# Optimization experiments

Measured on AMD Instinct MI355X. Metric: run time of the kernel, lower is better.

The kernel has to match this reference:

```python
import jax, jax.numpy as jnp
import numpy as np

DIM = 768
HEADS = 12
HEAD_DIM = DIM // HEADS
SCALE = HEAD_DIM ** -0.5
B = 8
N = 2121   # 1 cls + 1600 + 400 + 100 + 20 text
NT = 20

# token ranges: cls [0,1), x0 [1,1601), x1 [1601,2001), x2 [2001,2101), t [2101,2121)
SLICES = {'cls': (0, 1), 'x0': (1, 1601), 'x1': (1601, 2001), 'x2': (2001, 2101), 't': (2101, 2121)}


def setup_inputs() -> dict:
    key = jax.random.key(0)
    k1, k2, k3, k4 = jax.random.split(key, 4)
    src = jax.random.normal(k1, (B, N, DIM), dtype=jnp.float32)
    visu_mask = jnp.zeros((B, 2101), dtype=bool)   # True = masked out
    text_mask = jnp.zeros((B, NT), dtype=bool)
    w_qkv = jax.random.normal(k2, (DIM, 3 * DIM), dtype=jnp.float32) * 0.02
    w_proj = jax.random.normal(k3, (DIM, DIM), dtype=jnp.float32) * 0.02
    b_proj = jax.random.normal(k4, (DIM,), dtype=jnp.float32) * 0.02
    return {'src': src, 'visu_mask': visu_mask, 'text_mask': text_mask,
            'w_qkv': w_qkv, 'w_proj': w_proj, 'b_proj': b_proj}


def _attn(q, k, v, mask):
    # q: [B,H,Nq,D], k/v: [B,H,Nk,D], mask: [B,Nk] bool (True = masked)
    scores = jnp.einsum('bhqd,bhkd->bhqk', q * SCALE, k)
    scores = jnp.where(mask[:, None, None, :], -jnp.inf, scores)
    p = jax.nn.softmax(scores, axis=-1)
    o = jnp.einsum('bhqk,bhkd->bhqd', p, v)          # [B,H,Nq,D]
    return o.transpose(0, 2, 1, 3).reshape(q.shape[0], q.shape[2], -1)  # [B,Nq,C]


def reference(src, visu_mask, text_mask, w_qkv, w_proj, b_proj):
    qkv = (src @ w_qkv).reshape(B, N, 3, HEADS, HEAD_DIM).transpose(2, 0, 3, 1, 4)
    q, k, v = qkv[0], qkv[1], qkv[2]                  # [B,H,N,D]

    def blk(t, lo, hi):
        return t[:, :, lo:hi, :]

    (c0, c1), (a0, a1), (b0, b1), (d0, d1), (t0, t1) = (
        SLICES['cls'], SLICES['x0'], SLICES['x1'], SLICES['x2'], SLICES['t'])

    x0_mask = visu_mask[:, a0:a1]
    x1_mask = visu_mask[:, b0:b1]
    x2_mask = visu_mask[:, d0:d1]
    full_mask = jnp.concatenate([visu_mask, text_mask], axis=1)   # [B, N]

    # cls attends to everything
    cls = _attn(blk(q, c0, c1), k, v, full_mask)
    # x2 attends to x0+x1+x2+t
    k_x2 = jnp.concatenate([blk(k, a0, a1), blk(k, b0, b1), blk(k, d0, d1), blk(k, t0, t1)], axis=2)
    v_x2 = jnp.concatenate([blk(v, a0, a1), blk(v, b0, b1), blk(v, d0, d1), blk(v, t0, t1)], axis=2)
    m_x2 = jnp.concatenate([x0_mask, x1_mask, x2_mask, text_mask], axis=1)
    x2 = _attn(blk(q, d0, d1), k_x2, v_x2, m_x2)
    # x1 attends to x0+x1+t
    k_x1 = jnp.concatenate([blk(k, a0, a1), blk(k, b0, b1), blk(k, t0, t1)], axis=2)
    v_x1 = jnp.concatenate([blk(v, a0, a1), blk(v, b0, b1), blk(v, t0, t1)], axis=2)
    m_x1 = jnp.concatenate([x0_mask, x1_mask, text_mask], axis=1)
    x1 = _attn(blk(q, b0, b1), k_x1, v_x1, m_x1)
    # x0 attends to x0+t
    k_x0 = jnp.concatenate([blk(k, a0, a1), blk(k, t0, t1)], axis=2)
    v_x0 = jnp.concatenate([blk(v, a0, a1), blk(v, t0, t1)], axis=2)
    m_x0 = jnp.concatenate([x0_mask, text_mask], axis=1)
    x0 = _attn(blk(q, a0, a1), k_x0, v_x0, m_x0)
    # text attends to everything
    t = _attn(blk(q, t0, t1), k, v, full_mask)

    x = jnp.concatenate([cls, x0, x1, x2, t], axis=1)
    return x @ w_proj + b_proj
```

## Files before the change

### kernel.cpp

```cpp
#include <hip/hip_runtime.h>
#include <stdint.h>

typedef short           bf16x8 __attribute__((ext_vector_type(8)));
typedef float           f32x4  __attribute__((ext_vector_type(4)));
typedef float           f32x16 __attribute__((ext_vector_type(16)));
typedef unsigned short  u16;
typedef u16             u16x8  __attribute__((ext_vector_type(8)));
typedef uint32_t        u32;
typedef unsigned long long u64;

#define NB    8
#define NSEQ  2121
#define NPAD  2176
#define MROWS 16968
#define MPAD  17024
#define NH    12

#if __has_builtin(__builtin_amdgcn_exp2f)
#define EXP2F(x) __builtin_amdgcn_exp2f(x)
#else
#define EXP2F(x) exp2f(x)
#endif

#define INVALID_S   (-90000.0f)

__device__ __forceinline__ u16 f2bf(float f) {
  uint32_t u = __float_as_uint(f);
  u += 0x7fffu + ((u >> 16) & 1u);
  return (u16)(u >> 16);
}

__global__ void transpose_cast(const float* __restrict__ in, u16* __restrict__ out,
                               int R, int C, int scale_cols, float scale)
{
  __shared__ float tile[32][33];
  const int c0 = blockIdx.x * 32, r0 = blockIdx.y * 32;
  const int tx = threadIdx.x, ty = threadIdx.y;
#pragma unroll
  for (int i = 0; i < 4; i++) {
    const int r = r0 + ty + i * 8;
    tile[ty + i * 8][tx] = in[(size_t)r * C + c0 + tx];
  }
  __syncthreads();
#pragma unroll
  for (int i = 0; i < 4; i++) {
    const int c = c0 + ty + i * 8;
    float v = tile[tx][ty + i * 8];
    if (c < scale_cols) v *= scale;
    out[(size_t)c * R + r0 + tx] = f2bf(v);
  }
}

__global__ __launch_bounds__(256) void cast_src_bf16(const float* __restrict__ in,
                                                     u16* __restrict__ out)
{
  const size_t i = ((size_t)blockIdx.x * 256 + threadIdx.x) * 8;
  float4 a = *(const float4*)(in + i);
  float4 b = *(const float4*)(in + i + 4);
  u16x8 t;
  t[0] = f2bf(a.x); t[1] = f2bf(a.y); t[2] = f2bf(a.z); t[3] = f2bf(a.w);
  t[4] = f2bf(b.x); t[5] = f2bf(b.y); t[6] = f2bf(b.z); t[7] = f2bf(b.w);
  *(u16x8*)(out + i) = t;
}

__global__ __launch_bounds__(256) void gemm_qkv_kernel(
    const u16* __restrict__ srcb, const u16* __restrict__ wt,
    u16* __restrict__ qk, u16* __restrict__ vt)
{
  __shared__ u16 As[128][40];
  __shared__ u16 Bs[128][40];
  const int tid  = threadIdx.x;
  const int lane = tid & 63, wave = tid >> 6;
  const int wr = wave >> 1, wc = wave & 1;
  const int col = lane & 15, grp = lane >> 4;
  const int m0 = blockIdx.y * 128, n0 = blockIdx.x * 128;
  const int arow = tid >> 1, akoff = (tid & 1) * 16;

  const f32x4 fz = {0.f, 0.f, 0.f, 0.f};
  f32x4 acc[4][4];
#pragma unroll
  for (int i = 0; i < 4; i++)
#pragma unroll
    for (int j = 0; j < 4; j++) acc[i][j] = fz;

  const u16* abase = srcb + (size_t)(m0 + arow) * 768 + akoff;
  const u16* bbase = wt   + (size_t)(n0 + arow) * 768 + akoff;
  u16x8 aa0, aa1, bb0, bb1;
  aa0 = *(const u16x8*)(abase);
  aa1 = *(const u16x8*)(abase + 8);
  bb0 = *(const u16x8*)(bbase);
  bb1 = *(const u16x8*)(bbase + 8);

  for (int kb = 0; kb < 768; kb += 32) {
    *(u16x8*)&As[arow][akoff]     = aa0;
    *(u16x8*)&As[arow][akoff + 8] = aa1;
    *(u16x8*)&Bs[arow][akoff]     = bb0;
    *(u16x8*)&Bs[arow][akoff + 8] = bb1;
    __syncthreads();

    if (kb + 32 < 768) {
      aa0 = *(const u16x8*)(abase + kb + 32);
      aa1 = *(const u16x8*)(abase + kb + 40);
      bb0 = *(const u16x8*)(bbase + kb + 32);
      bb1 = *(const u16x8*)(bbase + kb + 40);
    }

    bf16x8 af[4], bfr[4];
#pragma unroll
    for (int mt = 0; mt < 4; mt++) af[mt]  = *(const bf16x8*)&As[wr * 64 + mt * 16 + col][grp * 8];
#pragma unroll
    for (int nt = 0; nt < 4; nt++) bfr[nt] = *(const bf16x8*)&Bs[wc * 64 + nt * 16 + col][grp * 8];
#pragma unroll
    for (int mt = 0; mt < 4; mt++)
#pragma unroll
      for (int nt = 0; nt < 4; nt++)
        acc[mt][nt] = __builtin_amdgcn_mfma_f32_16x16x32_bf16(af[mt], bfr[nt], acc[mt][nt], 0, 0, 0);
    __syncthreads();
  }

#pragma unroll
  for (int mt = 0; mt < 4; mt++) {
#pragma unroll
    for (int r = 0; r < 4; r++) {
      const int mm = m0 + wr * 64 + mt * 16 + grp * 4 + r;
      if (mm >= MROWS) continue;
      const uint32_t bb = (uint32_t)mm / 2121u;
      const uint32_t nn = (uint32_t)mm - bb * 2121u;
#pragma unroll
      for (int nt = 0; nt < 4; nt++) {
        const int c = n0 + wc * 64 + nt * 16 + col;
        const u16 bits = f2bf(acc[mt][nt][r]);
        if (c < 1536) {
          qk[(size_t)mm * 1536 + c] = bits;
        } else {
          const int hd = c - 1536;
          const int h = hd >> 6, d = hd & 63;
          vt[((size_t)(bb * NH + h) * 64 + d) * NPAD + nn] = bits;
        }
      }
    }
  }
}

__global__ __launch_bounds__(256) void gemm_proj_kernel(
    const u16* __restrict__ A, const u16* __restrict__ Bt,
    const float* __restrict__ bias, float* __restrict__ out)
{
  __shared__ u16 As[128][40];
  __shared__ u16 Bs[128][40];
  const int tid  = threadIdx.x;
  const int lane = tid & 63, wave = tid >> 6;
  const int wr = wave >> 1, wc = wave & 1;
  const int col = lane & 15, grp = lane >> 4;
  const int m0 = blockIdx.y * 128, n0 = blockIdx.x * 128;
  const int arow = tid >> 1, akoff = (tid & 1) * 16;

  const f32x4 fz = {0.f, 0.f, 0.f, 0.f};
  f32x4 acc[4][4];
#pragma unroll
  for (int i = 0; i < 4; i++)
#pragma unroll
    for (int j = 0; j < 4; j++) acc[i][j] = fz;

  const u16* abase = A  + (size_t)(m0 + arow) * 768 + akoff;
  const u16* bbase = Bt + (size_t)(n0 + arow) * 768 + akoff;
  u16x8 aa0, aa1, bb0, bb1;
  aa0 = *(const u16x8*)(abase);
  aa1 = *(const u16x8*)(abase + 8);
  bb0 = *(const u16x8*)(bbase);
  bb1 = *(const u16x8*)(bbase + 8);

  for (int kb = 0; kb < 768; kb += 32) {
    *(u16x8*)&As[arow][akoff]     = aa0;
    *(u16x8*)&As[arow][akoff + 8] = aa1;
    *(u16x8*)&Bs[arow][akoff]     = bb0;
    *(u16x8*)&Bs[arow][akoff + 8] = bb1;
    __syncthreads();

    if (kb + 32 < 768) {
      aa0 = *(const u16x8*)(abase + kb + 32);
      aa1 = *(const u16x8*)(abase + kb + 40);
      bb0 = *(const u16x8*)(bbase + kb + 32);
      bb1 = *(const u16x8*)(bbase + kb + 40);
    }

    bf16x8 af[4], bfr[4];
#pragma unroll
    for (int mt = 0; mt < 4; mt++) af[mt]  = *(const bf16x8*)&As[wr * 64 + mt * 16 + col][grp * 8];
#pragma unroll
    for (int nt = 0; nt < 4; nt++) bfr[nt] = *(const bf16x8*)&Bs[wc * 64 + nt * 16 + col][grp * 8];
#pragma unroll
    for (int mt = 0; mt < 4; mt++)
#pragma unroll
      for (int nt = 0; nt < 4; nt++)
        acc[mt][nt] = __builtin_amdgcn_mfma_f32_16x16x32_bf16(af[mt], bfr[nt], acc[mt][nt], 0, 0, 0);
    __syncthreads();
  }

#pragma unroll
  for (int mt = 0; mt < 4; mt++) {
#pragma unroll
    for (int r = 0; r < 4; r++) {
      const int mm = m0 + wr * 64 + mt * 16 + grp * 4 + r;
      if (mm >= MROWS) continue;
#pragma unroll
      for (int nt = 0; nt < 4; nt++) {
        const int c = n0 + wc * 64 + nt * 16 + col;
        out[(size_t)mm * 768 + c] = acc[mt][nt][r] + bias[c];
      }
    }
  }
}

__global__ __launch_bounds__(512) void attn_kernel(
    const u16* __restrict__ qkbuf, const u16* __restrict__ vt,
    const unsigned char* __restrict__ visu, const unsigned char* __restrict__ text,
    u16* __restrict__ attnout)
{
  __shared__ __align__(16) u16 Ks[2][64][72];
  __shared__ __align__(16) u16 Vs[2][64][72];
  __shared__ __align__(16) u64 mb64[34];
  __shared__ __align__(16) float lduf[8][32];

  const int tid  = threadIdx.x;
  const int lane = tid & 63, wave = tid >> 6;
  const int l31 = lane & 31, h = lane >> 5;

  const int fid = blockIdx.x;
  const int swz = (fid & 7) * 108 + (fid >> 3);
  const int qtile = swz % 9;
  const int bh = swz / 9;
  const int b = bh / NH, hh = bh % NH;
  const int qt0 = qtile * 256;
  const int q0 = qt0 + wave * 32;
  const int qrow = q0 + l31;

  for (int c = wave; c < 34; c += 8) {
    const int key = c * 64 + lane;
    int mb = 1;
    if (key < 2101)      mb = visu[b * 2101 + key] ? 1 : 0;
    else if (key < 2121) mb = text[b * 20 + (key - 2101)] ? 1 : 0;
    const u64 bal = __ballot(mb != 0);
    if (lane == 0) mb64[c] = bal;
  }

  const int qload = (qrow < NSEQ) ? qrow : (NSEQ - 1);
  bf16x8 qf[4];
  {
    const u16* qp = qkbuf + (size_t)(b * NSEQ + qload) * 1536 + hh * 64 + h * 8;
#pragma unroll
    for (int s = 0; s < 4; s++) qf[s] = *(const bf16x8*)(qp + s * 16);
  }

  int ks, ke, ex;
  if (qrow == 0)        { ks = 0; ke = 2121; ex = 0; }
  else if (qrow < 1601) { ks = 1; ke = 1601; ex = 1; }
  else if (qrow < 2001) { ks = 1; ke = 2001; ex = 1; }
  else if (qrow < 2101) { ks = 1; ke = 2121; ex = 0; }
  else if (qrow < 2121) { ks = 0; ke = 2121; ex = 0; }
  else                  { ks = 0; ke = 0;    ex = 0; }

  const int hi = (qt0 + 255 < 2120) ? (qt0 + 255) : 2120;
  int ke_tile, extra;
  if (qt0 == 0 || hi >= 2001) { ke_tile = 2121; extra = 0; }
  else if (hi >= 1601)        { ke_tile = 2001; extra = 1; }
  else                        { ke_tile = 1601; extra = 1; }
  const int nkv = (ke_tile + 63) >> 6;
  const int ntot = nkv + extra;

  f32x16 O0, O1;
#pragma unroll
  for (int i = 0; i < 16; i++) { O0[i] = 0.f; O1[i] = 0.f; }
  float lrun = 0.f;

  const int srow = tid >> 3, skoff = (tid & 7) * 8;
  const size_t vbase = (size_t)(b * NH + hh) * 64 * NPAD;
  const u16* kbase = qkbuf + (size_t)(b * NSEQ + srow) * 1536 + 768 + hh * 64 + skoff;
  const u16* vrow  = vt + vbase + (size_t)srow * NPAD + skoff;

  *(u16x8*)&Ks[0][srow][skoff] = *(const u16x8*)kbase;
  *(u16x8*)&Vs[0][srow][skoff] = *(const u16x8*)vrow;
  __syncthreads();

  u16x8 kpre, vpre;

  for (int it = 0; it < ntot; ++it) {
    const int cur = it & 1;
    const int kv0 = (it < nkv) ? it * 64 : 2096;
    const bool more = (it + 1 < ntot);

    if (more) {
      const int kvn = (it + 1 < nkv) ? (it + 1) * 64 : 2096;
      kpre = *(const u16x8*)(kbase + (size_t)kvn * 1536);
      vpre = *(const u16x8*)(vrow + kvn);
    }

    const int skipl = (kv0 >= ke) && !((ex != 0) && (kv0 < 2121) && (kv0 + 64 > 2101));
    if (!__all(skipl)) {
      f32x16 S0, S1;
#pragma unroll
      for (int i = 0; i < 16; i++) { S0[i] = 0.f; S1[i] = 0.f; }
      __builtin_amdgcn_s_setprio(1);
#pragma unroll
      for (int s = 0; s < 4; s++) {
        const bf16x8 k0 = *(const bf16x8*)&Ks[cur][l31][s * 16 + h * 8];
        const bf16x8 k1 = *(const bf16x8*)&Ks[cur][32 + l31][s * 16 + h * 8];
        S0 = __builtin_amdgcn_mfma_f32_32x32x16_bf16(k0, qf[s], S0, 0, 0, 0);
        S1 = __builtin_amdgcn_mfma_f32_32x32x16_bf16(k1, qf[s], S1, 0, 0, 0);
      }
      __builtin_amdgcn_s_setprio(0);

      const int fastl = (kv0 >= ks) && (kv0 + 64 <= ke);
      const u64 mword = (it < nkv) ? mb64[it] : ((mb64[32] >> 48) | (mb64[33] << 16));
      const bool plain = __all(fastl) && (mword == 0ull);
      if (!plain) {
        const u32 wlo = (u32)mword, whi = (u32)(mword >> 32);
#pragma unroll
        for (int m = 0; m < 4; m++) {
#pragma unroll
          for (int r = 0; r < 4; r++) {
            const int bitpos = 8 * m + 4 * h + r;
            {
              const int key = kv0 + bitpos;
              bool valid = ((key >= ks) && (key < ke)) || ((ex != 0) && (key >= 2101));
              valid = valid && (((wlo >> bitpos) & 1u) == 0u);
              S0[4 * m + r] = valid ? S0[4 * m + r] : INVALID_S;
            }
            {
              const int key = kv0 + 32 + bitpos;
              bool valid = ((key >= ks) && (key < ke)) || ((ex != 0) && (key >= 2101));
              valid = valid && (((whi >> bitpos) & 1u) == 0u);
              S1[4 * m + r] = valid ? S1[4 * m + r] : INVALID_S;
            }
          }
        }
      }

      float ls = 0.f;
#pragma unroll
      for (int i = 0; i < 16; i++) { const float p = EXP2F(S0[i]); S0[i] = p; ls += p; }
#pragma unroll
      for (int i = 0; i < 16; i++) { const float p = EXP2F(S1[i]); S1[i] = p; ls += p; }
      lrun += ls;

      bf16x8 pa[4];
      {
        u32 w[8];
#pragma unroll
        for (int j = 0; j < 8; j++) {
          u32 t;
          asm("v_cvt_pk_bf16_f32 %0, %1, %2" : "=v"(t) : "v"(S0[2 * j]), "v"(S0[2 * j + 1]));
          w[j] = t;
        }
        asm("v_permlane32_swap_b32 %0, %1" : "+v"(w[0]), "+v"(w[2]));
        asm("v_permlane32_swap_b32 %0, %1" : "+v"(w[1]), "+v"(w[3]));
        asm("v_permlane32_swap_b32 %0, %1" : "+v"(w[4]), "+v"(w[6]));
        asm("v_permlane32_swap_b32 %0, %1" : "+v"(w[5]), "+v"(w[7]));
        union { u32 u[4]; bf16x8 v; } f0, f1;
        f0.u[0] = w[0]; f0.u[1] = w[1]; f0.u[2] = w[2]; f0.u[3] = w[3];
        f1.u[0] = w[4]; f1.u[1] = w[5]; f1.u[2] = w[6]; f1.u[3] = w[7];
        pa[0] = f0.v; pa[1] = f1.v;
      }
      {
        u32 w[8];
#pragma unroll
        for (int j = 0; j < 8; j++) {
          u32 t;
          asm("v_cvt_pk_bf16_f32 %0, %1, %2" : "=v"(t) : "v"(S1[2 * j]), "v"(S1[2 * j + 1]));
          w[j] = t;
        }
        asm("v_permlane32_swap_b32 %0, %1" : "+v"(w[0]), "+v"(w[2]));
        asm("v_permlane32_swap_b32 %0, %1" : "+v"(w[1]), "+v"(w[3]));
        asm("v_permlane32_swap_b32 %0, %1" : "+v"(w[4]), "+v"(w[6]));
        asm("v_permlane32_swap_b32 %0, %1" : "+v"(w[5]), "+v"(w[7]));
        union { u32 u[4]; bf16x8 v; } f0, f1;
        f0.u[0] = w[0]; f0.u[1] = w[1]; f0.u[2] = w[2]; f0.u[3] = w[3];
        f1.u[0] = w[4]; f1.u[1] = w[5]; f1.u[2] = w[6]; f1.u[3] = w[7];
        pa[2] = f0.v; pa[3] = f1.v;
      }

      __builtin_amdgcn_s_setprio(1);
#pragma unroll
      for (int ck = 0; ck < 4; ck++) {
        const bf16x8 vf0 = *(const bf16x8*)&Vs[cur][l31][ck * 16 + h * 8];
        const bf16x8 vf1 = *(const bf16x8*)&Vs[cur][32 + l31][ck * 16 + h * 8];
        O0 = __builtin_amdgcn_mfma_f32_32x32x16_bf16(pa[ck], vf0, O0, 0, 0, 0);
        O1 = __builtin_amdgcn_mfma_f32_32x32x16_bf16(pa[ck], vf1, O1, 0, 0, 0);
      }
      __builtin_amdgcn_s_setprio(0);
    }

    if (more) {
      *(u16x8*)&Ks[cur ^ 1][srow][skoff] = kpre;
      *(u16x8*)&Vs[cur ^ 1][srow][skoff] = vpre;
    }
    __syncthreads();
  }

  float ltot = lrun + __shfl_xor(lrun, 32);
  if (h == 0) lduf[wave][l31] = ltot;
#pragma unroll
  for (int m = 0; m < 4; m++) {
    const f32x4 lv = *(const f32x4*)&lduf[wave][8 * m + 4 * h];
#pragma unroll
    for (int r = 0; r < 4; r++) {
      const float linv = (lv[r] > 0.f) ? 1.0f / lv[r] : 0.f;
      const int n = q0 + 8 * m + 4 * h + r;
      if (n >= NSEQ) continue;
      u16* op = attnout + (size_t)(b * NSEQ + n) * 768 + hh * 64 + l31;
      op[0]  = f2bf(O0[4 * m + r] * linv);
      op[32] = f2bf(O1[4 * m + r] * linv);
    }
  }
}

extern "C" void kernel_launch(void* const* d_in, const int* in_sizes, int n_in,
                              void* d_out, int out_size, void* d_ws, size_t ws_size,
                              hipStream_t stream) {
  const float* src  = (const float*)d_in[0];
  const unsigned char* visu = (const unsigned char*)d_in[1];
  const unsigned char* text = (const unsigned char*)d_in[2];
  const float* w_qkv = (const float*)d_in[3];
  const float* w_proj = (const float*)d_in[4];
  const float* b_proj = (const float*)d_in[5];
  float* out = (float*)d_out;

  char* ws = (char*)d_ws;
  size_t off = 0;
  auto alloc = [&](size_t bytes) { char* p = ws + off; off += (bytes + 255) & ~(size_t)255; return p; };
  u16* wqkv_t  = (u16*)alloc((size_t)2304 * 768 * 2);
  u16* wproj_t = (u16*)alloc((size_t)768 * 768 * 2);
  u16* qk      = (u16*)alloc((size_t)MPAD * 1536 * 2);
  u16* vtb     = (u16*)alloc((size_t)NB * NH * 64 * NPAD * 2);
  u16* tmp0    = (u16*)alloc((size_t)MPAD * 768 * 2);
  (void)ws_size; (void)in_sizes; (void)n_in; (void)out_size;

  transpose_cast<<<dim3(2304 / 32, 768 / 32), dim3(32, 8), 0, stream>>>(w_qkv, wqkv_t, 768, 2304, 768, 0.125f * 1.4426950408889634f);
  transpose_cast<<<dim3(768 / 32, 768 / 32), dim3(32, 8), 0, stream>>>(w_proj, wproj_t, 768, 768, 0, 1.0f);
  cast_src_bf16<<<dim3(6363), dim3(256), 0, stream>>>(src, tmp0);
  gemm_qkv_kernel<<<dim3(18, 133), dim3(256), 0, stream>>>(tmp0, wqkv_t, qk, vtb);
  attn_kernel<<<dim3(864), dim3(512), 0, stream>>>(qk, vtb, visu, text, tmp0);
  gemm_proj_kernel<<<dim3(6, 133), dim3(256), 0, stream>>>(tmp0, wproj_t, b_proj, out);
}
```

Baseline: 391.8 us.

## Load K/V fragments directly from global per wave, dropping LDS staging

```diff
diff --git a/kernel.cpp b/kernel.cpp
--- a/kernel.cpp
+++ b/kernel.cpp
@@ -212,30 +212,28 @@
   }
 }
 
-__global__ __launch_bounds__(512) void attn_kernel(
+__global__ __launch_bounds__(256) void attn_kernel(
     const u16* __restrict__ qkbuf, const u16* __restrict__ vt,
     const unsigned char* __restrict__ visu, const unsigned char* __restrict__ text,
     u16* __restrict__ attnout)
 {
-  __shared__ __align__(16) u16 Ks[2][64][72];
-  __shared__ __align__(16) u16 Vs[2][64][72];
   __shared__ __align__(16) u64 mb64[34];
-  __shared__ __align__(16) float lduf[8][32];
+  __shared__ __align__(16) float lduf[4][32];
 
   const int tid  = threadIdx.x;
   const int lane = tid & 63, wave = tid >> 6;
   const int l31 = lane & 31, h = lane >> 5;
 
   const int fid = blockIdx.x;
-  const int swz = (fid & 7) * 108 + (fid >> 3);
-  const int qtile = swz % 9;
-  const int bh = swz / 9;
+  const int swz = (fid & 7) * 204 + (fid >> 3);
+  const int qtile = swz % 17;
+  const int bh = swz / 17;
   const int b = bh / NH, hh = bh % NH;
-  const int qt0 = qtile * 256;
+  const int qt0 = qtile * 128;
   const int q0 = qt0 + wave * 32;
   const int qrow = q0 + l31;
 
-  for (int c = wave; c < 34; c += 8) {
+  for (int c = wave; c < 34; c += 4) {
     const int key = c * 64 + lane;
     int mb = 1;
     if (key < 2101)      mb = visu[b * 2101 + key] ? 1 : 0;
@@ -243,11 +241,11 @@
     const u64 bal = __ballot(mb != 0);
     if (lane == 0) mb64[c] = bal;
   }
-
-  const int qload = (qrow < NSEQ) ? qrow : (NSEQ - 1);
+  __syncthreads();
+
   bf16x8 qf[4];
   {
-    const u16* qp = qkbuf + (size_t)(b * NSEQ + qload) * 1536 + hh * 64 + h * 8;
+    const u16* qp = qkbuf + (size_t)(b * NSEQ + qrow) * 1536 + hh * 64 + h * 8;
 #pragma unroll
     for (int s = 0; s < 4; s++) qf[s] = *(const bf16x8*)(qp + s * 16);
   }
@@ -260,141 +258,133 @@
   else if (qrow < 2121) { ks = 0; ke = 2121; ex = 0; }
   else                  { ks = 0; ke = 0;    ex = 0; }
 
-  const int hi = (qt0 + 255 < 2120) ? (qt0 + 255) : 2120;
-  int ke_tile, extra;
-  if (qt0 == 0 || hi >= 2001) { ke_tile = 2121; extra = 0; }
-  else if (hi >= 1601)        { ke_tile = 2001; extra = 1; }
-  else                        { ke_tile = 1601; extra = 1; }
-  const int nkv = (ke_tile + 63) >> 6;
-  const int ntot = nkv + extra;
+  int ntot, nkv;
+  if (q0 >= NSEQ) {
+    ntot = 0; nkv = 0;
+  } else {
+    const int hi = (q0 + 31 < 2120) ? (q0 + 31) : 2120;
+    int ke_tile, extra;
+    if (q0 == 0 || hi >= 2001) { ke_tile = 2121; extra = 0; }
+    else if (hi >= 1601)       { ke_tile = 2001; extra = 1; }
+    else                       { ke_tile = 1601; extra = 1; }
+    nkv = (ke_tile + 63) >> 6;
+    ntot = nkv + extra;
+  }
 
   f32x16 O0, O1;
 #pragma unroll
   for (int i = 0; i < 16; i++) { O0[i] = 0.f; O1[i] = 0.f; }
   float lrun = 0.f;
 
-  const int srow = tid >> 3, skoff = (tid & 7) * 8;
-  const size_t vbase = (size_t)(b * NH + hh) * 64 * NPAD;
-  const u16* kbase = qkbuf + (size_t)(b * NSEQ + srow) * 1536 + 768 + hh * 64 + skoff;
-  const u16* vrow  = vt + vbase + (size_t)srow * NPAD + skoff;
-
-  *(u16x8*)&Ks[0][srow][skoff] = *(const u16x8*)kbase;
-  *(u16x8*)&Vs[0][srow][skoff] = *(const u16x8*)vrow;
-  __syncthreads();
-
-  u16x8 kpre, vpre;
+  const u16* kp0 = qkbuf + (size_t)(b * NSEQ + l31) * 1536 + 768 + hh * 64 + h * 8;
+  const u16* vp0 = vt + (size_t)(b * NH + hh) * 64 * NPAD + (size_t)l31 * NPAD + h * 8;
 
   for (int it = 0; it < ntot; ++it) {
-    const int cur = it & 1;
     const int kv0 = (it < nkv) ? it * 64 : 2096;
-    const bool more = (it + 1 < ntot);
-
-    if (more) {
-      const int kvn = (it + 1 < nkv) ? (it + 1) * 64 : 2096;
-      kpre = *(const u16x8*)(kbase + (size_t)kvn * 1536);
-      vpre = *(const u16x8*)(vrow + kvn);
-    }
-
-    const int skipl = (kv0 >= ke) && !((ex != 0) && (kv0 < 2121) && (kv0 + 64 > 2101));
-    if (!__all(skipl)) {
-      f32x16 S0, S1;
-#pragma unroll
-      for (int i = 0; i < 16; i++) { S0[i] = 0.f; S1[i] = 0.f; }
-      __builtin_amdgcn_s_setprio(1);
-#pragma unroll
-      for (int s = 0; s < 4; s++) {
-        const bf16x8 k0 = *(const bf16x8*)&Ks[cur][l31][s * 16 + h * 8];
-        const bf16x8 k1 = *(const bf16x8*)&Ks[cur][32 + l31][s * 16 + h * 8];
-        S0 = __builtin_amdgcn_mfma_f32_32x32x16_bf16(k0, qf[s], S0, 0, 0, 0);
-        S1 = __builtin_amdgcn_mfma_f32_32x32x16_bf16(k1, qf[s], S1, 0, 0, 0);
-      }
-      __builtin_amdgcn_s_setprio(0);
-
-      const int fastl = (kv0 >= ks) && (kv0 + 64 <= ke);
-      const u64 mword = (it < nkv) ? mb64[it] : ((mb64[32] >> 48) | (mb64[33] << 16));
-      const bool plain = __all(fastl) && (mword == 0ull);
-      if (!plain) {
-        const u32 wlo = (u32)mword, whi = (u32)(mword >> 32);
-#pragma unroll
-        for (int m = 0; m < 4; m++) {
-#pragma unroll
-          for (int r = 0; r < 4; r++) {
-            const int bitpos = 8 * m + 4 * h + r;
-            {
-              const int key = kv0 + bitpos;
-              bool valid = ((key >= ks) && (key < ke)) || ((ex != 0) && (key >= 2101));
-              valid = valid && (((wlo >> bitpos) & 1u) == 0u);
-              S0[4 * m + r] = valid ? S0[4 * m + r] : INVALID_S;
-            }
-            {
-              const int key = kv0 + 32 + bitpos;
-              bool valid = ((key >= ks) && (key < ke)) || ((ex != 0) && (key >= 2101));
-              valid = valid && (((whi >> bitpos) & 1u) == 0u);
-              S1[4 * m + r] = valid ? S1[4 * m + r] : INVALID_S;
-            }
+
+    const u16* kp = kp0 + (size_t)kv0 * 1536;
+    bf16x8 kf0[4], kf1[4];
+#pragma unroll
+    for (int s = 0; s < 4; s++) {
+      kf0[s] = *(const bf16x8*)(kp + s * 16);
+      kf1[s] = *(const bf16x8*)(kp + (size_t)32 * 1536 + s * 16);
+    }
+
+    f32x16 S0, S1;
+#pragma unroll
+    for (int i = 0; i < 16; i++) { S0[i] = 0.f; S1[i] = 0.f; }
+    __builtin_amdgcn_s_setprio(1);
+#pragma unroll
+    for (int s = 0; s < 4; s++) {
+      S0 = __builtin_amdgcn_mfma_f32_32x32x16_bf16(kf0[s], qf[s], S0, 0, 0, 0);
+      S1 = __builtin_amdgcn_mfma_f32_32x32x16_bf16(kf1[s], qf[s], S1, 0, 0, 0);
+    }
+    __builtin_amdgcn_s_setprio(0);
+
+    const u16* vp = vp0 + kv0;
+    bf16x8 vf0[4], vf1[4];
+#pragma unroll
+    for (int ck = 0; ck < 4; ck++) {
+      vf0[ck] = *(const bf16x8*)(vp + ck * 16);
+      vf1[ck] = *(const bf16x8*)(vp + (size_t)32 * NPAD + ck * 16);
+    }
+
+    const int fastl = (kv0 >= ks) && (kv0 + 64 <= ke);
+    const u64 mword = (it < nkv) ? mb64[it] : ((mb64[32] >> 48) | (mb64[33] << 16));
+    const bool plain = __all(fastl) && (mword == 0ull);
+    if (!plain) {
+      const u32 wlo = (u32)mword, whi = (u32)(mword >> 32);
+#pragma unroll
+      for (int m = 0; m < 4; m++) {
+#pragma unroll
+        for (int r = 0; r < 4; r++) {
+          const int bitpos = 8 * m + 4 * h + r;
+          {
+            const int key = kv0 + bitpos;
+            bool valid = ((key >= ks) && (key < ke)) || ((ex != 0) && (key >= 2101));
+            valid = valid && (((wlo >> bitpos) & 1u) == 0u);
+            S0[4 * m + r] = valid ? S0[4 * m + r] : INVALID_S;
+          }
+          {
+            const int key = kv0 + 32 + bitpos;
+            bool valid = ((key >= ks) && (key < ke)) || ((ex != 0) && (key >= 2101));
+            valid = valid && (((whi >> bitpos) & 1u) == 0u);
+            S1[4 * m + r] = valid ? S1[4 * m + r] : INVALID_S;
           }
         }
       }
-
-      float ls = 0.f;
-#pragma unroll
-      for (int i = 0; i < 16; i++) { const float p = EXP2F(S0[i]); S0[i] = p; ls += p; }
-#pragma unroll
-      for (int i = 0; i < 16; i++) { const float p = EXP2F(S1[i]); S1[i] = p; ls += p; }
-      lrun += ls;
-
-      bf16x8 pa[4];
-      {
-        u32 w[8];
-#pragma unroll
-        for (int j = 0; j < 8; j++) {
-          u32 t;
-          asm("v_cvt_pk_bf16_f32 %0, %1, %2" : "=v"(t) : "v"(S0[2 * j]), "v"(S0[2 * j + 1]));
-          w[j] = t;
-        }
-        asm("v_permlane32_swap_b32 %0, %1" : "+v"(w[0]), "+v"(w[2]));
-        asm("v_permlane32_swap_b32 %0, %1" : "+v"(w[1]), "+v"(w[3]));
-        asm("v_permlane32_swap_b32 %0, %1" : "+v"(w[4]), "+v"(w[6]));
-        asm("v_permlane32_swap_b32 %0, %1" : "+v"(w[5]), "+v"(w[7]));
-        union { u32 u[4]; bf16x8 v; } f0, f1;
-        f0.u[0] = w[0]; f0.u[1] = w[1]; f0.u[2] = w[2]; f0.u[3] = w[3];
-        f1.u[0] = w[4]; f1.u[1] = w[5]; f1.u[2] = w[6]; f1.u[3] = w[7];
-        pa[0] = f0.v; pa[1] = f1.v;
+    }
+
+    float ls = 0.f;
+#pragma unroll
+    for (int i = 0; i < 16; i++) { const float p = EXP2F(S0[i]); S0[i] = p; ls += p; }
+#pragma unroll
+    for (int i = 0; i < 16; i++) { const float p = EXP2F(S1[i]); S1[i] = p; ls += p; }
+    lrun += ls;
+
+    bf16x8 pa[4];
+    {
+      u32 w[8];
+#pragma unroll
+      for (int j = 0; j < 8; j++) {
+        u32 t;
+        asm("v_cvt_pk_bf16_f32 %0, %1, %2" : "=v"(t) : "v"(S0[2 * j]), "v"(S0[2 * j + 1]));
+        w[j] = t;
       }
-      {
-        u32 w[8];
-#pragma unroll
-        for (int j = 0; j < 8; j++) {
-          u32 t;
-          asm("v_cvt_pk_bf16_f32 %0, %1, %2" : "=v"(t) : "v"(S1[2 * j]), "v"(S1[2 * j + 1]));
-          w[j] = t;
-        }
-        asm("v_permlane32_swap_b32 %0, %1" : "+v"(w[0]), "+v"(w[2]));
-        asm("v_permlane32_swap_b32 %0, %1" : "+v"(w[1]), "+v"(w[3]));
-        asm("v_permlane32_swap_b32 %0, %1" : "+v"(w[4]), "+v"(w[6]));
-        asm("v_permlane32_swap_b32 %0, %1" : "+v"(w[5]), "+v"(w[7]));
-        union { u32 u[4]; bf16x8 v; } f0, f1;
-        f0.u[0] = w[0]; f0.u[1] = w[1]; f0.u[2] = w[2]; f0.u[3] = w[3];
-        f1.u[0] = w[4]; f1.u[1] = w[5]; f1.u[2] = w[6]; f1.u[3] = w[7];
-        pa[2] = f0.v; pa[3] = f1.v;
+      asm("v_permlane32_swap_b32 %0, %1" : "+v"(w[0]), "+v"(w[2]));
+      asm("v_permlane32_swap_b32 %0, %1" : "+v"(w[1]), "+v"(w[3]));
+      asm("v_permlane32_swap_b32 %0, %1" : "+v"(w[4]), "+v"(w[6]));
+      asm("v_permlane32_swap_b32 %0, %1" : "+v"(w[5]), "+v"(w[7]));
+      union { u32 u[4]; bf16x8 v; } f0, f1;
+      f0.u[0] = w[0]; f0.u[1] = w[1]; f0.u[2] = w[2]; f0.u[3] = w[3];
+      f1.u[0] = w[4]; f1.u[1] = w[5]; f1.u[2] = w[6]; f1.u[3] = w[7];
+      pa[0] = f0.v; pa[1] = f1.v;
+    }
+    {
+      u32 w[8];
+#pragma unroll
+      for (int j = 0; j < 8; j++) {
+        u32 t;
+        asm("v_cvt_pk_bf16_f32 %0, %1, %2" : "=v"(t) : "v"(S1[2 * j]), "v"(S1[2 * j + 1]));
+        w[j] = t;
       }
-
-      __builtin_amdgcn_s_setprio(1);
-#pragma unroll
-      for (int ck = 0; ck < 4; ck++) {
-        const bf16x8 vf0 = *(const bf16x8*)&Vs[cur][l31][ck * 16 + h * 8];
-        const bf16x8 vf1 = *(const bf16x8*)&Vs[cur][32 + l31][ck * 16 + h * 8];
-        O0 = __builtin_amdgcn_mfma_f32_32x32x16_bf16(pa[ck], vf0, O0, 0, 0, 0);
-        O1 = __builtin_amdgcn_mfma_f32_32x32x16_bf16(pa[ck], vf1, O1, 0, 0, 0);
-      }
-      __builtin_amdgcn_s_setprio(0);
-    }
-
-    if (more) {
-      *(u16x8*)&Ks[cur ^ 1][srow][skoff] = kpre;
-      *(u16x8*)&Vs[cur ^ 1][srow][skoff] = vpre;
-    }
-    __syncthreads();
+      asm("v_permlane32_swap_b32 %0, %1" : "+v"(w[0]), "+v"(w[2]));
+      asm("v_permlane32_swap_b32 %0, %1" : "+v"(w[1]), "+v"(w[3]));
+      asm("v_permlane32_swap_b32 %0, %1" : "+v"(w[4]), "+v"(w[6]));
+      asm("v_permlane32_swap_b32 %0, %1" : "+v"(w[5]), "+v"(w[7]));
+      union { u32 u[4]; bf16x8 v; } f0, f1;
+      f0.u[0] = w[0]; f0.u[1] = w[1]; f0.u[2] = w[2]; f0.u[3] = w[3];
+      f1.u[0] = w[4]; f1.u[1] = w[5]; f1.u[2] = w[6]; f1.u[3] = w[7];
+      pa[2] = f0.v; pa[3] = f1.v;
+    }
+
+    __builtin_amdgcn_s_setprio(1);
+#pragma unroll
+    for (int ck = 0; ck < 4; ck++) {
+      O0 = __builtin_amdgcn_mfma_f32_32x32x16_bf16(pa[ck], vf0[ck], O0, 0, 0, 0);
+      O1 = __builtin_amdgcn_mfma_f32_32x32x16_bf16(pa[ck], vf1[ck], O1, 0, 0, 0);
+    }
+    __builtin_amdgcn_s_setprio(0);
   }
 
   float ltot = lrun + __shfl_xor(lrun, 32);
@@ -439,6 +429,6 @@
   transpose_cast<<<dim3(768 / 32, 768 / 32), dim3(32, 8), 0, stream>>>(w_proj, wproj_t, 768, 768, 0, 1.0f);
   cast_src_bf16<<<dim3(6363), dim3(256), 0, stream>>>(src, tmp0);
   gemm_qkv_kernel<<<dim3(18, 133), dim3(256), 0, stream>>>(tmp0, wqkv_t, qk, vtb);
-  attn_kernel<<<dim3(864), dim3(512), 0, stream>>>(qk, vtb, visu, text, tmp0);
+  attn_kernel<<<dim3(1632), dim3(256), 0, stream>>>(qk, vtb, visu, text, tmp0);
   gemm_proj_kernel<<<dim3(6, 133), dim3(256), 0, stream>>>(tmp0, wproj_t, b_proj, out);
 }
```

After: 581.2 us. +48.3%, slower.
